# Performance work log

Hardware: AMD Instinct MI355X
Metric: run time of the kernel (lower is better)

Reference implementation:

```python
import jax, jax.numpy as jnp
import numpy as np

IN_CH, OUT_CH, KS = 64, 128, 3
GRID, DEG = 8, 3
STRIDE, PAD = 1, 1
SIZE = IN_CH * KS * KS            # 576
NCOEF = GRID + DEG                # 11
GRID_RANGE = (-1.0, 1.0)


def _xavier_uniform(key, shape):
    fan_out, fan_in = shape
    a = float(np.sqrt(6.0 / (fan_in + fan_out)))
    return jax.random.uniform(key, shape, minval=-a, maxval=a, dtype=jnp.float32)


def setup_inputs() -> dict:
    key = jax.random.key(0)
    k1, k2, k3 = jax.random.split(key, 3)
    x = jax.random.normal(k1, (8, IN_CH, 32, 32), dtype=jnp.float32)
    # non-trainable knot grid, one row per unfolded feature
    knots = jnp.tile(jnp.linspace(GRID_RANGE[0], GRID_RANGE[1], GRID + 1, dtype=jnp.float32)[None, :], (SIZE, 1))
    coeff = 0.1 * jax.random.normal(k2, (OUT_CH, SIZE, NCOEF), dtype=jnp.float32)
    base_weights = _xavier_uniform(k3, (OUT_CH, SIZE))
    spline_weights = jnp.ones((OUT_CH, SIZE), dtype=jnp.float32)
    return {"x": x, "knots": knots, "coeff": coeff,
            "base_weights": base_weights, "spline_weights": spline_weights}


def bspline_basis(x, grid, k):
    # x: (S, P) evaluation points; grid: (S, G+1) knots. Returns (S, G+k, P).
    h = (grid[:, -1:] - grid[:, :1]) / (grid.shape[1] - 1)
    left = grid[:, :1] - h * jnp.arange(k, 0, -1, dtype=x.dtype)
    right = grid[:, -1:] + h * jnp.arange(1, k + 1, dtype=x.dtype)
    g = jnp.concatenate([left, grid, right], axis=1)  # (S, G+1+2k)
    xe = x[:, None, :]
    B = ((xe >= g[:, :-1, None]) & (xe < g[:, 1:, None])).astype(x.dtype)
    for d in range(1, k + 1):  # de Boor recursion over fixed degree
        B = ((xe - g[:, :-(d + 1), None]) / (g[:, d:-1, None] - g[:, :-(d + 1), None]) * B[:, :-1]
             + (g[:, d + 1:, None] - xe) / (g[:, d + 1:, None] - g[:, 1:-d, None]) * B[:, 1:])
    return B


def _unfold(x):
    # torch F.unfold with channel-major (c, kh, kw) feature ordering
    N, C, H, W = x.shape
    xp = jnp.pad(x, ((0, 0), (0, 0), (PAD, PAD), (PAD, PAD)))
    Hp = (H + 2 * PAD - KS) // STRIDE + 1
    Wp = (W + 2 * PAD - KS) // STRIDE + 1
    patches = jnp.stack([xp[:, :, i:i + STRIDE * Hp:STRIDE, j:j + STRIDE * Wp:STRIDE]
                         for i in range(KS) for j in range(KS)], axis=2)  # (N, C, KS*KS, Hp, Wp)
    L = Hp * Wp
    u = patches.reshape(N, SIZE, L)              # (N, size, L)
    u = jnp.transpose(u, (1, 0, 2)).reshape(SIZE, N * L)  # (size, N*L), col = n*L + l
    return u, Hp, Wp


def reference(x, knots, coeff, base_weights, spline_weights):
    N = x.shape[0]
    u, Hp, Wp = _unfold(x)                                   # (size, P)
    base = base_weights @ jax.nn.silu(u)                     # (Cout, P)
    B = bspline_basis(u, knots, DEG)                         # (size, ncoef, P)
    eff = spline_weights[:, :, None] * coeff                 # (Cout, size, ncoef)
    spl = jnp.einsum('csj,sjp->cp', eff, B)                  # (Cout, P)
    out = (base + spl).reshape(OUT_CH, N, Hp, Wp)
    return jnp.transpose(out, (1, 0, 2, 3))                  # (N, Cout, Hp, Wp)
```

## Files before the change

### kernel.cpp

```cpp
#include <hip/hip_runtime.h>


typedef __attribute__((ext_vector_type(8))) short bf16x8;
typedef __attribute__((ext_vector_type(4))) float f32x4;
typedef __attribute__((ext_vector_type(4))) unsigned short u16x4;

#define WSWZ_BYTES 1769472
#define PART_OFF   WSWZ_BYTES

__device__ __forceinline__ short f2bf(float f) {
    union { float f; unsigned u; } c; c.f = f;
    unsigned r = c.u + 0x7fffu + ((c.u >> 16) & 1u);
    return (short)(r >> 16);
}
__device__ __forceinline__ float bf2f(unsigned short u) {
    union { unsigned u; float f; } c; c.u = ((unsigned)u) << 16;
    return c.f;
}

__global__ void kan_weights(const float* __restrict__ coeff,
                            const float* __restrict__ basew,
                            const float* __restrict__ splw,
                            short* __restrict__ Wswz) {
    __shared__ float coeffL[6336];
    __shared__ float basewL[576];
    __shared__ float splwL[576];
    const int co = blockIdx.x;
    const int t  = threadIdx.x;
    const float* crow = coeff + co * 6336;
    for (int i = t; i < 6336; i += 256) coeffL[i] = crow[i];
    for (int i = t; i < 576; i += 256) {
        basewL[i] = basew[co * 576 + i];
        splwL[i]  = splw[co * 576 + i];
    }
    __syncthreads();
    const int cb = co >> 4, lm = co & 15;
    for (int c = t; c < 864; c += 256) {
        int kk = c >> 2, quad = c & 3;
        int f  = kk / 18;
        int rm = kk - f * 18;
        int tap = rm >> 1, ks = rm & 1;
        bf16x8 pack;
#pragma unroll
        for (int j = 0; j < 8; ++j) {
            int ci = ks * 32 + quad * 8 + j;
            int s  = ci * 9 + tap;
            float v = (f == 0) ? basewL[s] : splwL[s] * coeffL[s * 11 + (f - 1)];
            pack[j] = f2bf(v);
        }
        *(bf16x8*)(Wswz + ((kk * 8 + cb) * 64 + quad * 16 + lm) * 8) = pack;
    }
}

__global__ __launch_bounds__(256, 2)
void kan_gemm(const float* __restrict__ x,
              const short* __restrict__ Wswz,
              float* __restrict__ part) {
    __shared__ unsigned short xs[4 * 64 * 36];
    __shared__ short Bs[3 * 8704];

    const int t    = threadIdx.x;
    const int w    = t >> 6;
    const int l    = t & 63;
    const int lp   = l & 15;
    const int quad = l >> 4;
    const int wm   = w >> 1;
    const int wn   = w & 1;

    const int bz    = blockIdx.x;
    const int fg    = bz & 3;
    const int ptile = bz >> 2;
    const int n     = ptile >> 4;
    const int y0    = (ptile & 15) << 1;

#pragma unroll
    for (int it = 0; it < 8; ++it) {
        int cg = t + it * 256;
        int rr = cg >> 9, ci = (cg >> 3) & 63, q = cg & 7;
        int y  = y0 - 1 + rr;
        f32x4 v = {0.f, 0.f, 0.f, 0.f};
        if (y >= 0 && y < 32)
            v = *(const f32x4*)(x + (((n * 64 + ci) * 32 + y) * 32 + q * 4));
        u16x4 p;
        p.x = (unsigned short)f2bf(v.x); p.y = (unsigned short)f2bf(v.y);
        p.z = (unsigned short)f2bf(v.z); p.w = (unsigned short)f2bf(v.w);
        *(u16x4*)&xs[(rr * 64 + ci) * 36 + q * 4] = p;
    }
    __syncthreads();

    const int f0 = fg * 3;
    for (int it = t; it < 1088; it += 256) {
        int rr  = it / 272;
        int rem = it - rr * 272;
        int xp = rem >> 3, cch = rem & 7, c0 = cch << 3;
        bool interior = (xp >= 1 && xp <= 32);
        bf16x8 packs[3];
#pragma unroll
        for (int j = 0; j < 8; ++j) {
            float v = interior ? bf2f(xs[(rr * 64 + c0 + j) * 36 + (xp - 1)]) : 0.f;
            float silu = v / (1.f + __expf(-v));
            float tt = 4.f * v + 7.f;
            int   i0 = -100;
            float b0 = 0.f, b1 = 0.f, b2 = 0.f, b3 = 0.f;
            if (tt >= 0.f && tt < 14.f) {
                i0 = (int)tt;
                float fr  = tt - (float)i0;
                float omf = 1.f - fr;
                float fr2 = fr * fr, fr3 = fr2 * fr;
                b0 = omf * omf * omf * (1.f / 6.f);
                b1 = (3.f * fr3 - 6.f * fr2 + 4.f) * (1.f / 6.f);
                b2 = (-3.f * fr3 + 3.f * fr2 + 3.f * fr + 1.f) * (1.f / 6.f);
                b3 = fr3 * (1.f / 6.f);
            }
#pragma unroll
            for (int p = 0; p < 3; ++p) {
                int f = f0 + p;
                float val;
                if (f == 0) val = silu;
                else {
                    int jj = f - 1;
                    val = 0.f;
                    val = (jj == i0 - 3) ? b0 : val;
                    val = (jj == i0 - 2) ? b1 : val;
                    val = (jj == i0 - 1) ? b2 : val;
                    val = (jj == i0    ) ? b3 : val;
                }
                packs[p][j] = f2bf(val);
            }
        }
        int pix = rr * 34 + xp;
        int swz = (cch ^ (pix & 7)) << 3;
#pragma unroll
        for (int p = 0; p < 3; ++p)
            *(bf16x8*)&Bs[p * 8704 + pix * 64 + swz] = packs[p];
    }
    __syncthreads();

    f32x4 acc[4][2];
#pragma unroll
    for (int m = 0; m < 4; ++m)
#pragma unroll
        for (int nt = 0; nt < 2; ++nt) {
            f32x4 z = {0.f, 0.f, 0.f, 0.f};
            acc[m][nt] = z;
        }

    const short* Ap = Wswz + (size_t)(f0 * 18) * 4096 + (wm * 4) * 512 + l * 8;
    bf16x8 an[4];
#pragma unroll
    for (int m = 0; m < 4; ++m)
        an[m] = *(const bf16x8*)(Ap + m * 512);

#pragma unroll 1
    for (int p = 0; p < 3; ++p) {
        const short* B0 = Bs + p * 8704;
#pragma unroll
        for (int kk = 0; kk < 18; ++kk) {
            bf16x8 ac[4];
#pragma unroll
            for (int m = 0; m < 4; ++m) ac[m] = an[m];
            Ap += 4096;
#pragma unroll
            for (int m = 0; m < 4; ++m)
                an[m] = *(const bf16x8*)(Ap + m * 512);

            const int tap = kk >> 1, ks = kk & 1;
            const int dy  = tap / 3;
            const int dx  = tap - dy * 3;
            const int c   = ks * 4 + quad;
#pragma unroll
            for (int nt = 0; nt < 2; ++nt) {
                int pix = (wn + dy) * 34 + (nt << 4) + lp + dx;
                bf16x8 b = *(const bf16x8*)&B0[pix * 64 + ((c ^ (pix & 7)) << 3)];
                acc[0][nt] = __builtin_amdgcn_mfma_f32_16x16x32_bf16(ac[0], b, acc[0][nt], 0, 0, 0);
                acc[1][nt] = __builtin_amdgcn_mfma_f32_16x16x32_bf16(ac[1], b, acc[1][nt], 0, 0, 0);
                acc[2][nt] = __builtin_amdgcn_mfma_f32_16x16x32_bf16(ac[2], b, acc[2][nt], 0, 0, 0);
                acc[3][nt] = __builtin_amdgcn_mfma_f32_16x16x32_bf16(ac[3], b, acc[3][nt], 0, 0, 0);
            }
        }
    }

    float* dst = part + (size_t)fg * 1048576;
#pragma unroll
    for (int m = 0; m < 4; ++m)
#pragma unroll
        for (int nt = 0; nt < 2; ++nt)
#pragma unroll
            for (int r = 0; r < 4; ++r) {
                int co = wm * 64 + m * 16 + quad * 4 + r;
                int y  = y0 + wn;
                int xx = (nt << 4) + lp;
                dst[((size_t)(n * 128 + co) * 32 + y) * 32 + xx] = acc[m][nt][r];
            }
}

__global__ void kan_reduce(const float* __restrict__ part,
                           float* __restrict__ out) {
    int g = blockIdx.x * 256 + threadIdx.x;
    f32x4 a = ((const f32x4*)part)[g];
#pragma unroll
    for (int s = 1; s < 4; ++s)
        a += ((const f32x4*)(part + (size_t)s * 1048576))[g];
    ((f32x4*)out)[g] = a;
}

extern "C" void kernel_launch(void* const* d_in, const int* in_sizes, int n_in,
                              void* d_out, int out_size, void* d_ws, size_t ws_size,
                              hipStream_t stream) {
    const float* x     = (const float*)d_in[0];
    const float* coeff = (const float*)d_in[2];
    const float* basew = (const float*)d_in[3];
    const float* splw  = (const float*)d_in[4];
    float* out = (float*)d_out;

    short* Wswz = (short*)d_ws;
    float* part = (float*)((char*)d_ws + PART_OFF);

    kan_weights<<<128, 256, 0, stream>>>(coeff, basew, splw, Wswz);
    kan_gemm<<<512, 256, 0, stream>>>(x, Wswz, part);
    kan_reduce<<<1024, 256, 0, stream>>>(part, out);
}
```

Before: 107.0 us.

## Switch GEMM to 32x32x16 MFMA with per-wave 32-channel output tiles

Replaces the 16x16x32 bf16 MFMA tiling (each wave 64 channels x 32 pixels over 4x2 tiles) with 32x32x16 MFMA where each wave owns 32 output channels and both pixel rows. The weight swizzle in the prep kernel is reorganized to match the new A-operand layout. The aim is fewer MFMA instructions and less A-operand fetch overhead per unit of work. In exchange, the software prefetch of the A fragments is removed, so each global weight load now sits directly in the MFMA dependency chain, and the number of B LDS reads per MFMA changes.

```diff
diff --git a/kernel.cpp b/kernel.cpp
--- a/kernel.cpp
+++ b/kernel.cpp
@@ -3,6 +3,7 @@
 
 typedef __attribute__((ext_vector_type(8))) short bf16x8;
 typedef __attribute__((ext_vector_type(4))) float f32x4;
+typedef __attribute__((ext_vector_type(16))) float f32x16;
 typedef __attribute__((ext_vector_type(4))) unsigned short u16x4;
 
 #define WSWZ_BYTES 1769472
@@ -34,21 +35,21 @@
         splwL[i]  = splw[co * 576 + i];
     }
     __syncthreads();
-    const int cb = co >> 4, lm = co & 15;
+    const int cb = co >> 5, lm = co & 31;
     for (int c = t; c < 864; c += 256) {
-        int kk = c >> 2, quad = c & 3;
-        int f  = kk / 18;
-        int rm = kk - f * 18;
-        int tap = rm >> 1, ks = rm & 1;
+        int kk16 = c >> 1, kh = c & 1;
+        int f  = kk16 / 36;
+        int rm = kk16 - f * 36;
+        int tap = rm >> 2, q = rm & 3;
         bf16x8 pack;
 #pragma unroll
         for (int j = 0; j < 8; ++j) {
-            int ci = ks * 32 + quad * 8 + j;
+            int ci = q * 16 + kh * 8 + j;
             int s  = ci * 9 + tap;
             float v = (f == 0) ? basewL[s] : splwL[s] * coeffL[s * 11 + (f - 1)];
             pack[j] = f2bf(v);
         }
-        *(bf16x8*)(Wswz + ((kk * 8 + cb) * 64 + quad * 16 + lm) * 8) = pack;
+        *(bf16x8*)(Wswz + (size_t)((kk16 * 4 + cb) * 64 + kh * 32 + lm) * 8) = pack;
     }
 }
 
@@ -59,13 +60,11 @@
     __shared__ unsigned short xs[4 * 64 * 36];
     __shared__ short Bs[3 * 8704];
 
-    const int t    = threadIdx.x;
-    const int w    = t >> 6;
-    const int l    = t & 63;
-    const int lp   = l & 15;
-    const int quad = l >> 4;
-    const int wm   = w >> 1;
-    const int wn   = w & 1;
+    const int t  = threadIdx.x;
+    const int w  = t >> 6;
+    const int l  = t & 63;
+    const int ln = l & 31;
+    const int kh = l >> 5;
 
     const int bz    = blockIdx.x;
     const int fg    = bz & 3;
@@ -136,62 +135,45 @@
     }
     __syncthreads();
 
-    f32x4 acc[4][2];
-#pragma unroll
-    for (int m = 0; m < 4; ++m)
-#pragma unroll
-        for (int nt = 0; nt < 2; ++nt) {
-            f32x4 z = {0.f, 0.f, 0.f, 0.f};
-            acc[m][nt] = z;
-        }
-
-    const short* Ap = Wswz + (size_t)(f0 * 18) * 4096 + (wm * 4) * 512 + l * 8;
-    bf16x8 an[4];
-#pragma unroll
-    for (int m = 0; m < 4; ++m)
-        an[m] = *(const bf16x8*)(Ap + m * 512);
-
+    f32x16 acc[2];
+#pragma unroll
+    for (int pb = 0; pb < 2; ++pb)
+#pragma unroll
+        for (int r = 0; r < 16; ++r)
+            acc[pb][r] = 0.f;
+
+    const short* Abase = Wswz + (size_t)w * 512 + (size_t)l * 8;
 #pragma unroll 1
     for (int p = 0; p < 3; ++p) {
         const short* B0 = Bs + p * 8704;
-#pragma unroll
-        for (int kk = 0; kk < 18; ++kk) {
-            bf16x8 ac[4];
-#pragma unroll
-            for (int m = 0; m < 4; ++m) ac[m] = an[m];
-            Ap += 4096;
-#pragma unroll
-            for (int m = 0; m < 4; ++m)
-                an[m] = *(const bf16x8*)(Ap + m * 512);
-
-            const int tap = kk >> 1, ks = kk & 1;
+        const int kbase = (f0 + p) * 36;
+#pragma unroll
+        for (int rm = 0; rm < 36; ++rm) {
+            const int tap = rm >> 2, q = rm & 3;
             const int dy  = tap / 3;
             const int dx  = tap - dy * 3;
-            const int c   = ks * 4 + quad;
-#pragma unroll
-            for (int nt = 0; nt < 2; ++nt) {
-                int pix = (wn + dy) * 34 + (nt << 4) + lp + dx;
+            bf16x8 a = *(const bf16x8*)(Abase + (size_t)(kbase + rm) * 2048);
+            const int c = q * 2 + kh;
+#pragma unroll
+            for (int pb = 0; pb < 2; ++pb) {
+                int pix = (pb + dy) * 34 + ln + dx;
                 bf16x8 b = *(const bf16x8*)&B0[pix * 64 + ((c ^ (pix & 7)) << 3)];
-                acc[0][nt] = __builtin_amdgcn_mfma_f32_16x16x32_bf16(ac[0], b, acc[0][nt], 0, 0, 0);
-                acc[1][nt] = __builtin_amdgcn_mfma_f32_16x16x32_bf16(ac[1], b, acc[1][nt], 0, 0, 0);
-                acc[2][nt] = __builtin_amdgcn_mfma_f32_16x16x32_bf16(ac[2], b, acc[2][nt], 0, 0, 0);
-                acc[3][nt] = __builtin_amdgcn_mfma_f32_16x16x32_bf16(ac[3], b, acc[3][nt], 0, 0, 0);
+                acc[pb] = __builtin_amdgcn_mfma_f32_32x32x16_bf16(a, b, acc[pb], 0, 0, 0);
             }
         }
     }
 
     float* dst = part + (size_t)fg * 1048576;
 #pragma unroll
-    for (int m = 0; m < 4; ++m)
-#pragma unroll
-        for (int nt = 0; nt < 2; ++nt)
-#pragma unroll
-            for (int r = 0; r < 4; ++r) {
-                int co = wm * 64 + m * 16 + quad * 4 + r;
-                int y  = y0 + wn;
-                int xx = (nt << 4) + lp;
-                dst[((size_t)(n * 128 + co) * 32 + y) * 32 + xx] = acc[m][nt][r];
-            }
+    for (int pb = 0; pb < 2; ++pb) {
+        int y = y0 + pb;
+#pragma unroll
+        for (int r = 0; r < 16; ++r) {
+            int row = (r & 3) + 8 * (r >> 2) + 4 * kh;
+            int co  = w * 32 + row;
+            dst[((size_t)(n * 128 + co) * 32 + y) * 32 + ln] = acc[pb][r];
+        }
+    }
 }
 
 __global__ void kan_reduce(const float* __restrict__ part,
```

Measured after the change: 106.9 us. About the same (-0.1%).
